# Kernel optimization log

Measured on AMD Instinct MI355X. Metric: run time of the kernel, lower is better.

The kernel has to match this reference:

```python
import jax, jax.numpy as jnp
import numpy as np

FEATURE_DIM = 1024
HEAD_NUM = 16
HIDDEN_DIM = FEATURE_DIM // HEAD_NUM


def setup_inputs() -> dict:
    key = jax.random.key(0)
    ks = jax.random.split(key, 12)
    B, S, D = 4, 2048, FEATURE_DIM
    s = 1.0 / np.sqrt(D)
    inp = {
        "query": jax.random.normal(ks[0], (B, S, D), jnp.float32),
        "key": jax.random.normal(ks[1], (B, S, D), jnp.float32),
        "value": jax.random.normal(ks[2], (B, S, D), jnp.float32),
        "mask": jax.random.randint(ks[3], (B, 1, 1, S), 0, 2, jnp.int32),
        "Wq": jax.random.normal(ks[4], (D, D), jnp.float32) * s,
        "bq": jnp.zeros((D,), jnp.float32),
        "Wk": jax.random.normal(ks[5], (D, D), jnp.float32) * s,
        "bk": jnp.zeros((D,), jnp.float32),
        "Wv": jax.random.normal(ks[6], (D, D), jnp.float32) * s,
        "bv": jnp.zeros((D,), jnp.float32),
        "Wo": jax.random.normal(ks[7], (D, D), jnp.float32) * s,
        "bo": jnp.zeros((D,), jnp.float32),
    }
    return inp


def reference(query, key, value, mask, Wq, bq, Wk, bk, Wv, bv, Wo, bo):
    B, Sq, D = query.shape
    H, Hd = HEAD_NUM, HIDDEN_DIM
    scale = jnp.sqrt(jnp.asarray(Hd, query.dtype))

    def split_heads(x):
        b, s, _ = x.shape
        return x.reshape(b, s, H, Hd).transpose(0, 2, 1, 3)  # [B,H,S,Hd]

    Q = split_heads(query @ Wq.T + bq)
    K = split_heads(key @ Wk.T + bk)
    V = split_heads(value @ Wv.T + bv)

    scores = jnp.einsum("bhqd,bhkd->bhqk", Q, K) / scale
    scores = jnp.where(mask == 0, jnp.asarray(-1e10, scores.dtype), scores)
    attn = jax.nn.softmax(scores, axis=-1)  # dropout p=0 -> identity
    h = jnp.einsum("bhqk,bhkd->bhqd", attn, V)
    h = h.transpose(0, 2, 1, 3).reshape(B, Sq, D)
    return h @ Wo.T + bo
```

## Files before the change

### kernel.cpp

```cpp
#include <hip/hip_runtime.h>
#include <hip/hip_bf16.h>
#include <cstdint>
#include <cstddef>

#define D_MODEL 1024
#define SEQ     2048
#define BATCH   4
#define NHEAD   16
#define HD      64
#define MROWS   (BATCH * SEQ)

typedef __attribute__((ext_vector_type(8))) short  short8;
typedef __attribute__((ext_vector_type(4))) float  floatx4;
typedef __attribute__((ext_vector_type(4))) unsigned short ushort4v;
typedef unsigned short u16;

__device__ __forceinline__ u16 f2bf(float x) {
    __hip_bfloat16 h = __float2bfloat16(x);
    return *(u16*)&h;
}

__device__ __forceinline__ void async_copy16(const u16* g, u16* l) {
    __builtin_amdgcn_global_load_lds(
        (const __attribute__((address_space(1))) void*)g,
        (__attribute__((address_space(3))) void*)l, 16, 0, 0);
}

__device__ __forceinline__ void cvt8(const float* s, u16* d, size_t i) {
    const float4 a = *(const float4*)(s + i);
    const float4 b = *(const float4*)(s + i + 4);
    short8 o;
    o[0] = (short)f2bf(a.x); o[1] = (short)f2bf(a.y);
    o[2] = (short)f2bf(a.z); o[3] = (short)f2bf(a.w);
    o[4] = (short)f2bf(b.x); o[5] = (short)f2bf(b.y);
    o[6] = (short)f2bf(b.z); o[7] = (short)f2bf(b.w);
    *(short8*)(d + i) = o;
}

__global__ __launch_bounds__(256) void cvt3(
    const float* __restrict__ s0, const float* __restrict__ s1,
    const float* __restrict__ s2,
    u16* __restrict__ d0, u16* __restrict__ d1, u16* __restrict__ d2)
{
    const float* s = blockIdx.y == 0 ? s0 : (blockIdx.y == 1 ? s1 : s2);
    u16*         d = blockIdx.y == 0 ? d0 : (blockIdx.y == 1 ? d1 : d2);
    cvt8(s, d, ((size_t)blockIdx.x * 256 + threadIdx.x) * 8);
}

__global__ __launch_bounds__(256) void cvt4(
    const float* __restrict__ s0, const float* __restrict__ s1,
    const float* __restrict__ s2, const float* __restrict__ s3,
    u16* __restrict__ d0, u16* __restrict__ d1,
    u16* __restrict__ d2, u16* __restrict__ d3)
{
    const float* s = blockIdx.y == 0 ? s0 : (blockIdx.y == 1 ? s1 :
                     (blockIdx.y == 2 ? s2 : s3));
    u16*         d = blockIdx.y == 0 ? d0 : (blockIdx.y == 1 ? d1 :
                     (blockIdx.y == 2 ? d2 : d3));
    cvt8(s, d, ((size_t)blockIdx.x * 256 + threadIdx.x) * 8);
}

template <int LAYOUT>
__global__ __launch_bounds__(256) void gemm_mfma(
    const u16* __restrict__ A,
    const u16* __restrict__ W,
    const float* __restrict__ bias,
    void* __restrict__ out)
{
    constexpr int K = D_MODEL;
    __shared__ __align__(16) u16 smem[16384];
    u16 (*As)[64] = (u16(*)[64])smem;
    u16 (*Ws)[64] = (u16(*)[64])(smem + 8192);

    const int bm = blockIdx.x * 128;
    const int bn = blockIdx.y * 128;
    const int t  = threadIdx.x;
    const int w  = t >> 6;
    const int l  = t & 63;
    const int li = l & 15;
    const int quad = l >> 4;
    const int wm = (w & 1) * 64;
    const int wn = (w >> 1) * 64;
    const int lrow = l >> 3;
    const int lcol = (l & 7) * 8;

    const u16* Ag = A + (size_t)bm * K;
    const u16* Wg = W + (size_t)bn * K;

    floatx4 acc[4][4];
    #pragma unroll
    for (int mi = 0; mi < 4; mi++)
        #pragma unroll
        for (int ni = 0; ni < 4; ni++) acc[mi][ni] = (floatx4){0.f,0.f,0.f,0.f};

    for (int kt = 0; kt < K; kt += 64) {
        __syncthreads();
        #pragma unroll
        for (int j = 0; j < 4; j++) {
            const int r = w * 32 + j * 8;
            async_copy16(Ag + (size_t)(r + lrow) * K + kt + lcol, &As[r][0]);
            async_copy16(Wg + (size_t)(r + lrow) * K + kt + lcol, &Ws[r][0]);
        }
        __syncthreads();

        #pragma unroll
        for (int ks = 0; ks < 2; ks++) {
            short8 af[4], bf[4];
            #pragma unroll
            for (int i = 0; i < 4; i++) {
                af[i] = *(const short8*)&As[wm + i * 16 + li][ks * 32 + quad * 8];
                bf[i] = *(const short8*)&Ws[wn + i * 16 + li][ks * 32 + quad * 8];
            }
            #pragma unroll
            for (int mi = 0; mi < 4; mi++)
                #pragma unroll
                for (int ni = 0; ni < 4; ni++)
                    acc[mi][ni] = __builtin_amdgcn_mfma_f32_16x16x32_bf16(
                        af[mi], bf[ni], acc[mi][ni], 0, 0, 0);
        }
    }

    if (LAYOUT == 3) {
        float* o = (float*)out;
        #pragma unroll
        for (int mi = 0; mi < 4; mi++)
            #pragma unroll
            for (int ni = 0; ni < 4; ni++) {
                const int c = bn + wn + ni * 16 + li;
                const float bz = bias[c];
                #pragma unroll
                for (int reg = 0; reg < 4; reg++) {
                    const int r = bm + wm + mi * 16 + quad * 4 + reg;
                    o[(size_t)r * D_MODEL + c] = acc[mi][ni][reg] + bz;
                }
            }
    } else if (LAYOUT == 0) {
        u16* o = (u16*)out;
        #pragma unroll
        for (int mi = 0; mi < 4; mi++)
            #pragma unroll
            for (int ni = 0; ni < 4; ni++) {
                const int c  = bn + wn + ni * 16 + li;
                const int h  = c >> 6;
                const int hd = c & 63;
                const float bz = bias[c];
                #pragma unroll
                for (int reg = 0; reg < 4; reg++) {
                    const int r = bm + wm + mi * 16 + quad * 4 + reg;
                    const int b = r >> 11;
                    const int s = r & (SEQ - 1);
                    o[(((size_t)(b * NHEAD + h) * SEQ) + s) * HD + hd] = f2bf(acc[mi][ni][reg] + bz);
                }
            }
    } else {
        u16 (*Ct)[128] = (u16(*)[128])smem;
        __syncthreads();
        #pragma unroll
        for (int mi = 0; mi < 4; mi++)
            #pragma unroll
            for (int ni = 0; ni < 4; ni++) {
                const int cl = wn + ni * 16 + li;
                const float bz = bias[bn + cl];
                #pragma unroll
                for (int reg = 0; reg < 4; reg++) {
                    const int rl = wm + mi * 16 + quad * 4 + reg;
                    Ct[cl][rl] = f2bf(acc[mi][ni][reg] + bz);
                }
            }
        __syncthreads();
        const int cl   = t >> 1;
        const int half = t & 1;
        const int cg = bn + cl;
        const int h  = cg >> 6;
        const int hd = cg & 63;
        const int b  = bm >> 11;
        const int s0 = (bm & (SEQ - 1)) + half * 64;
        u16* dst = (u16*)out + (((size_t)(b * NHEAD + h) * HD) + hd) * SEQ + s0;
        const short8* sp = (const short8*)&Ct[cl][half * 64];
        #pragma unroll
        for (int i = 0; i < 8; i++) ((short8*)dst)[i] = sp[i];
    }
}

#define LOG2E   1.44269504088896340736f
#define CSCALE  (0.125f * LOG2E)

__global__ __launch_bounds__(256) void attn_mfma(
    const u16* __restrict__ Q,
    const u16* __restrict__ K,
    const u16* __restrict__ Vt,
    const int* __restrict__ mask,
    u16* __restrict__ H)
{
    __shared__ __align__(16) u16 Ks[64 * 64];
    __shared__ __align__(16) u16 Vs[64 * 64];
    __shared__ __align__(16) u16 Ps[4][32][72];
    __shared__ float mc[64];

    const int bh  = blockIdx.y;
    const int b   = bh >> 4;
    const int h   = bh & 15;
    const int q0  = blockIdx.x * 128;
    const int t   = threadIdx.x;
    const int w   = t >> 6;
    const int l   = t & 63;
    const int li  = l & 15;
    const int quad  = l >> 4;
    const int lrow8 = l >> 3;
    const int gch   = (l & 7) ^ lrow8;
    const int swz   = li & 7;

    short8 qf[2][2];
    #pragma unroll
    for (int qb = 0; qb < 2; qb++) {
        const u16* Qrow = Q + ((size_t)bh * SEQ + q0 + w * 32 + qb * 16 + li) * HD;
        qf[qb][0] = *(const short8*)(Qrow + quad * 8);
        qf[qb][1] = *(const short8*)(Qrow + 32 + quad * 8);
    }

    const u16* Kbh = K  + (size_t)bh * SEQ * HD;
    const u16* Vbh = Vt + (size_t)bh * HD * SEQ;
    const int* mg  = mask + (size_t)b * SEQ;

    floatx4 oacc[4][2];
    #pragma unroll
    for (int hm = 0; hm < 4; hm++)
        #pragma unroll
        for (int qb = 0; qb < 2; qb++) oacc[hm][qb] = (floatx4){0.f,0.f,0.f,0.f};
    float rs[2] = {0.f, 0.f};

    for (int kt = 0; kt < SEQ; kt += 64) {
        __syncthreads();
        #pragma unroll
        for (int j = 0; j < 2; j++) {
            const int rb = w * 16 + j * 8;
            async_copy16(Kbh + (size_t)(kt + rb + lrow8) * HD + gch * 8, &Ks[rb * 64]);
            async_copy16(Vbh + (size_t)(rb + lrow8) * SEQ + kt + gch * 8, &Vs[rb * 64]);
        }
        if (t < 64) mc[t] = (mg[kt + t] != 0) ? -16.0f : -1.0e9f;
        __syncthreads();

        floatx4 sacc[4][2];
        #pragma unroll
        for (int kb = 0; kb < 4; kb++)
            #pragma unroll
            for (int qb = 0; qb < 2; qb++) sacc[kb][qb] = (floatx4){0.f,0.f,0.f,0.f};
        #pragma unroll
        for (int ks = 0; ks < 2; ks++) {
            short8 kf[4];
            #pragma unroll
            for (int kb = 0; kb < 4; kb++)
                kf[kb] = *(const short8*)&Ks[(kb * 16 + li) * 64 + ((ks * 4 + quad) ^ swz) * 8];
            #pragma unroll
            for (int kb = 0; kb < 4; kb++)
                #pragma unroll
                for (int qb = 0; qb < 2; qb++)
                    sacc[kb][qb] = __builtin_amdgcn_mfma_f32_16x16x32_bf16(
                        kf[kb], qf[qb][ks], sacc[kb][qb], 0, 0, 0);
        }

        #pragma unroll
        for (int kb = 0; kb < 4; kb++) {
            const float4 m4 = *(const float4*)&mc[kb * 16 + quad * 4];
            #pragma unroll
            for (int qb = 0; qb < 2; qb++) {
                const float p0 = __builtin_amdgcn_exp2f(fmaf(sacc[kb][qb][0], CSCALE, m4.x));
                const float p1 = __builtin_amdgcn_exp2f(fmaf(sacc[kb][qb][1], CSCALE, m4.y));
                const float p2 = __builtin_amdgcn_exp2f(fmaf(sacc[kb][qb][2], CSCALE, m4.z));
                const float p3 = __builtin_amdgcn_exp2f(fmaf(sacc[kb][qb][3], CSCALE, m4.w));
                rs[qb] += (p0 + p1) + (p2 + p3);
                ushort4v pk;
                pk[0] = f2bf(p0); pk[1] = f2bf(p1);
                pk[2] = f2bf(p2); pk[3] = f2bf(p3);
                *(ushort4v*)&Ps[w][qb * 16 + li][kb * 16 + quad * 4] = pk;
            }
        }

        #pragma unroll
        for (int ks = 0; ks < 2; ks++) {
            short8 pf[2];
            #pragma unroll
            for (int qb = 0; qb < 2; qb++)
                pf[qb] = *(const short8*)&Ps[w][qb * 16 + li][ks * 32 + quad * 8];
            #pragma unroll
            for (int hm = 0; hm < 4; hm++) {
                const short8 vf = *(const short8*)&Vs[(hm * 16 + li) * 64 + ((ks * 4 + quad) ^ swz) * 8];
                #pragma unroll
                for (int qb = 0; qb < 2; qb++)
                    oacc[hm][qb] = __builtin_amdgcn_mfma_f32_16x16x32_bf16(
                        vf, pf[qb], oacc[hm][qb], 0, 0, 0);
            }
        }
    }

    float linv[2];
    #pragma unroll
    for (int qb = 0; qb < 2; qb++) {
        float v = rs[qb];
        v += __shfl_xor(v, 16, 64);
        v += __shfl_xor(v, 32, 64);
        linv[qb] = 1.0f / v;
    }
    #pragma unroll
    for (int qb = 0; qb < 2; qb++) {
        const size_t row = (size_t)b * SEQ + q0 + w * 32 + qb * 16 + li;
        #pragma unroll
        for (int hm = 0; hm < 4; hm++) {
            ushort4v o;
            #pragma unroll
            for (int reg = 0; reg < 4; reg++)
                o[reg] = f2bf(oacc[hm][qb][reg] * linv[qb]);
            *(ushort4v*)&H[row * D_MODEL + h * 64 + hm * 16 + quad * 4] = o;
        }
    }
}

extern "C" void kernel_launch(void* const* d_in, const int* in_sizes, int n_in,
                              void* d_out, int out_size, void* d_ws, size_t ws_size,
                              hipStream_t stream)
{
    const float* query = (const float*)d_in[0];
    const float* key_  = (const float*)d_in[1];
    const float* value = (const float*)d_in[2];
    const int*   mask  = (const int*)  d_in[3];
    const float* Wq = (const float*)d_in[4];
    const float* bq = (const float*)d_in[5];
    const float* Wk = (const float*)d_in[6];
    const float* bk = (const float*)d_in[7];
    const float* Wv = (const float*)d_in[8];
    const float* bv = (const float*)d_in[9];
    const float* Wo = (const float*)d_in[10];
    const float* bo = (const float*)d_in[11];
    float* out = (float*)d_out;

    const size_t per = (size_t)BATCH * NHEAD * SEQ * HD;
    const size_t wsz = (size_t)D_MODEL * D_MODEL;
    u16* qb  = (u16*)d_ws;
    u16* kb  = qb  + per;
    u16* vb  = kb  + per;
    u16* Qb  = vb  + per;
    u16* Kb  = Qb  + per;
    u16* Vtb = Kb  + per;
    u16* Hb  = Vtb + per;
    u16* Wqb = Hb  + per;
    u16* Wkb = Wqb + wsz;
    u16* Wvb = Wkb + wsz;
    u16* Wob = Wvb + wsz;

    cvt3<<<dim3(per / 2048, 3), 256, 0, stream>>>(query, key_, value, qb, kb, vb);
    cvt4<<<dim3(wsz / 2048, 4), 256, 0, stream>>>(Wq, Wk, Wv, Wo, Wqb, Wkb, Wvb, Wob);

    const dim3 gg(MROWS / 128, D_MODEL / 128);
    gemm_mfma<0><<<gg, 256, 0, stream>>>(qb, Wqb, bq, Qb);
    gemm_mfma<0><<<gg, 256, 0, stream>>>(kb, Wkb, bk, Kb);
    gemm_mfma<1><<<gg, 256, 0, stream>>>(vb, Wvb, bv, Vtb);

    attn_mfma<<<dim3(SEQ / 128, BATCH * NHEAD), 256, 0, stream>>>(
        Qb, Kb, Vtb, mask, Hb);

    gemm_mfma<3><<<gg, 256, 0, stream>>>(Hb, Wob, bo, out);
}
```

Measured before the change: 393.2 us.

## Fuse fp32-to-bf16 input conversion into batched QKV GEMM and double-buffer attention K/V

Drops the separate activation conversion kernel. The Q, K and V projections now run as one batched launch over blockIdx.z, and each reads fp32 activations directly, converting them to bf16 in registers with a register-prefetch software pipeline. The attention kernel double-buffers the K/V tiles and mask in LDS so the next tile's async loads overlap the current compute, and it drops one barrier per iteration. The goal is to remove a full round trip of activation traffic and two launches, and to hide load latency in attention. The cost is more LDS in attention and register-based loads instead of direct-to-LDS copies in the GEMM.

```diff
diff --git a/kernel.cpp b/kernel.cpp
--- a/kernel.cpp
+++ b/kernel.cpp
@@ -35,16 +35,6 @@
     o[4] = (short)f2bf(b.x); o[5] = (short)f2bf(b.y);
     o[6] = (short)f2bf(b.z); o[7] = (short)f2bf(b.w);
     *(short8*)(d + i) = o;
-}
-
-__global__ __launch_bounds__(256) void cvt3(
-    const float* __restrict__ s0, const float* __restrict__ s1,
-    const float* __restrict__ s2,
-    u16* __restrict__ d0, u16* __restrict__ d1, u16* __restrict__ d2)
-{
-    const float* s = blockIdx.y == 0 ? s0 : (blockIdx.y == 1 ? s1 : s2);
-    u16*         d = blockIdx.y == 0 ? d0 : (blockIdx.y == 1 ? d1 : d2);
-    cvt8(s, d, ((size_t)blockIdx.x * 256 + threadIdx.x) * 8);
 }
 
 __global__ __launch_bounds__(256) void cvt4(
@@ -60,12 +50,148 @@
     cvt8(s, d, ((size_t)blockIdx.x * 256 + threadIdx.x) * 8);
 }
 
-template <int LAYOUT>
-__global__ __launch_bounds__(256) void gemm_mfma(
+__global__ __launch_bounds__(256) void gemm_qkv(
+    const float* __restrict__ Aq, const float* __restrict__ Ak,
+    const float* __restrict__ Av,
+    const u16* __restrict__ Wqp, const u16* __restrict__ Wkp,
+    const u16* __restrict__ Wvp,
+    const float* __restrict__ bqp, const float* __restrict__ bkp,
+    const float* __restrict__ bvp,
+    u16* __restrict__ oq, u16* __restrict__ ok, u16* __restrict__ ov)
+{
+    constexpr int K = D_MODEL;
+    __shared__ __align__(16) u16 smem[16384];
+    u16 (*As)[64] = (u16(*)[64])smem;
+    u16 (*Ws)[64] = (u16(*)[64])(smem + 8192);
+
+    const int z = blockIdx.z;
+    const float* A    = z == 0 ? Aq  : (z == 1 ? Ak  : Av);
+    const u16*   W    = z == 0 ? Wqp : (z == 1 ? Wkp : Wvp);
+    const float* bias = z == 0 ? bqp : (z == 1 ? bkp : bvp);
+    u16*         out  = z == 0 ? oq  : (z == 1 ? ok  : ov);
+
+    const int bm = blockIdx.x * 128;
+    const int bn = blockIdx.y * 128;
+    const int t  = threadIdx.x;
+    const int w  = t >> 6;
+    const int l  = t & 63;
+    const int li = l & 15;
+    const int quad = l >> 4;
+    const int wm = (w & 1) * 64;
+    const int wn = (w >> 1) * 64;
+    const int srow = w * 32 + (l >> 3);
+    const int lc8  = (l & 7) * 8;
+
+    const float* Ab = A + (size_t)bm * K;
+    const u16*   Wb = W + (size_t)bn * K;
+
+    float4 pa[4][2];
+    short8 pw[4];
+    #pragma unroll
+    for (int j = 0; j < 4; j++) {
+        const float* ap = Ab + (size_t)(srow + j * 8) * K + lc8;
+        pa[j][0] = *(const float4*)ap;
+        pa[j][1] = *(const float4*)(ap + 4);
+        pw[j] = *(const short8*)(Wb + (size_t)(srow + j * 8) * K + lc8);
+    }
+
+    floatx4 acc[4][4];
+    #pragma unroll
+    for (int mi = 0; mi < 4; mi++)
+        #pragma unroll
+        for (int ni = 0; ni < 4; ni++) acc[mi][ni] = (floatx4){0.f,0.f,0.f,0.f};
+
+    for (int kt = 0; kt < K; kt += 64) {
+        __syncthreads();
+        #pragma unroll
+        for (int j = 0; j < 4; j++) {
+            short8 av;
+            av[0] = (short)f2bf(pa[j][0].x); av[1] = (short)f2bf(pa[j][0].y);
+            av[2] = (short)f2bf(pa[j][0].z); av[3] = (short)f2bf(pa[j][0].w);
+            av[4] = (short)f2bf(pa[j][1].x); av[5] = (short)f2bf(pa[j][1].y);
+            av[6] = (short)f2bf(pa[j][1].z); av[7] = (short)f2bf(pa[j][1].w);
+            *(short8*)&As[srow + j * 8][lc8] = av;
+            *(short8*)&Ws[srow + j * 8][lc8] = pw[j];
+        }
+        __syncthreads();
+        if (kt + 64 < K) {
+            #pragma unroll
+            for (int j = 0; j < 4; j++) {
+                const float* ap = Ab + (size_t)(srow + j * 8) * K + kt + 64 + lc8;
+                pa[j][0] = *(const float4*)ap;
+                pa[j][1] = *(const float4*)(ap + 4);
+                pw[j] = *(const short8*)(Wb + (size_t)(srow + j * 8) * K + kt + 64 + lc8);
+            }
+        }
+        #pragma unroll
+        for (int ks = 0; ks < 2; ks++) {
+            short8 af[4], bf[4];
+            #pragma unroll
+            for (int i = 0; i < 4; i++) {
+                af[i] = *(const short8*)&As[wm + i * 16 + li][ks * 32 + quad * 8];
+                bf[i] = *(const short8*)&Ws[wn + i * 16 + li][ks * 32 + quad * 8];
+            }
+            #pragma unroll
+            for (int mi = 0; mi < 4; mi++)
+                #pragma unroll
+                for (int ni = 0; ni < 4; ni++)
+                    acc[mi][ni] = __builtin_amdgcn_mfma_f32_16x16x32_bf16(
+                        af[mi], bf[ni], acc[mi][ni], 0, 0, 0);
+        }
+    }
+
+    if (z < 2) {
+        #pragma unroll
+        for (int mi = 0; mi < 4; mi++)
+            #pragma unroll
+            for (int ni = 0; ni < 4; ni++) {
+                const int c  = bn + wn + ni * 16 + li;
+                const int h  = c >> 6;
+                const int hd = c & 63;
+                const float bz = bias[c];
+                #pragma unroll
+                for (int reg = 0; reg < 4; reg++) {
+                    const int r = bm + wm + mi * 16 + quad * 4 + reg;
+                    const int b = r >> 11;
+                    const int s = r & (SEQ - 1);
+                    out[(((size_t)(b * NHEAD + h) * SEQ) + s) * HD + hd] = f2bf(acc[mi][ni][reg] + bz);
+                }
+            }
+    } else {
+        u16 (*Ct)[128] = (u16(*)[128])smem;
+        __syncthreads();
+        #pragma unroll
+        for (int mi = 0; mi < 4; mi++)
+            #pragma unroll
+            for (int ni = 0; ni < 4; ni++) {
+                const int cl = wn + ni * 16 + li;
+                const float bz = bias[bn + cl];
+                #pragma unroll
+                for (int reg = 0; reg < 4; reg++) {
+                    const int rl = wm + mi * 16 + quad * 4 + reg;
+                    Ct[cl][rl] = f2bf(acc[mi][ni][reg] + bz);
+                }
+            }
+        __syncthreads();
+        const int cl   = t >> 1;
+        const int half = t & 1;
+        const int cg = bn + cl;
+        const int h  = cg >> 6;
+        const int hd = cg & 63;
+        const int b  = bm >> 11;
+        const int s0 = (bm & (SEQ - 1)) + half * 64;
+        u16* dst = out + (((size_t)(b * NHEAD + h) * HD) + hd) * SEQ + s0;
+        const short8* sp = (const short8*)&Ct[cl][half * 64];
+        #pragma unroll
+        for (int i = 0; i < 8; i++) ((short8*)dst)[i] = sp[i];
+    }
+}
+
+__global__ __launch_bounds__(256) void gemm_out(
     const u16* __restrict__ A,
     const u16* __restrict__ W,
     const float* __restrict__ bias,
-    void* __restrict__ out)
+    float* __restrict__ out)
 {
     constexpr int K = D_MODEL;
     __shared__ __align__(16) u16 smem[16384];
@@ -120,66 +246,18 @@
         }
     }
 
-    if (LAYOUT == 3) {
-        float* o = (float*)out;
-        #pragma unroll
-        for (int mi = 0; mi < 4; mi++)
-            #pragma unroll
-            for (int ni = 0; ni < 4; ni++) {
-                const int c = bn + wn + ni * 16 + li;
-                const float bz = bias[c];
-                #pragma unroll
-                for (int reg = 0; reg < 4; reg++) {
-                    const int r = bm + wm + mi * 16 + quad * 4 + reg;
-                    o[(size_t)r * D_MODEL + c] = acc[mi][ni][reg] + bz;
-                }
-            }
-    } else if (LAYOUT == 0) {
-        u16* o = (u16*)out;
-        #pragma unroll
-        for (int mi = 0; mi < 4; mi++)
-            #pragma unroll
-            for (int ni = 0; ni < 4; ni++) {
-                const int c  = bn + wn + ni * 16 + li;
-                const int h  = c >> 6;
-                const int hd = c & 63;
-                const float bz = bias[c];
-                #pragma unroll
-                for (int reg = 0; reg < 4; reg++) {
-                    const int r = bm + wm + mi * 16 + quad * 4 + reg;
-                    const int b = r >> 11;
-                    const int s = r & (SEQ - 1);
-                    o[(((size_t)(b * NHEAD + h) * SEQ) + s) * HD + hd] = f2bf(acc[mi][ni][reg] + bz);
-                }
-            }
-    } else {
-        u16 (*Ct)[128] = (u16(*)[128])smem;
-        __syncthreads();
-        #pragma unroll
-        for (int mi = 0; mi < 4; mi++)
-            #pragma unroll
-            for (int ni = 0; ni < 4; ni++) {
-                const int cl = wn + ni * 16 + li;
-                const float bz = bias[bn + cl];
-                #pragma unroll
-                for (int reg = 0; reg < 4; reg++) {
-                    const int rl = wm + mi * 16 + quad * 4 + reg;
-                    Ct[cl][rl] = f2bf(acc[mi][ni][reg] + bz);
-                }
-            }
-        __syncthreads();
-        const int cl   = t >> 1;
-        const int half = t & 1;
-        const int cg = bn + cl;
-        const int h  = cg >> 6;
-        const int hd = cg & 63;
-        const int b  = bm >> 11;
-        const int s0 = (bm & (SEQ - 1)) + half * 64;
-        u16* dst = (u16*)out + (((size_t)(b * NHEAD + h) * HD) + hd) * SEQ + s0;
-        const short8* sp = (const short8*)&Ct[cl][half * 64];
-        #pragma unroll
-        for (int i = 0; i < 8; i++) ((short8*)dst)[i] = sp[i];
-    }
+    #pragma unroll
+    for (int mi = 0; mi < 4; mi++)
+        #pragma unroll
+        for (int ni = 0; ni < 4; ni++) {
+            const int c = bn + wn + ni * 16 + li;
+            const float bz = bias[c];
+            #pragma unroll
+            for (int reg = 0; reg < 4; reg++) {
+                const int r = bm + wm + mi * 16 + quad * 4 + reg;
+                out[(size_t)r * D_MODEL + c] = acc[mi][ni][reg] + bz;
+            }
+        }
 }
 
 #define LOG2E   1.44269504088896340736f
@@ -192,10 +270,10 @@
     const int* __restrict__ mask,
     u16* __restrict__ H)
 {
-    __shared__ __align__(16) u16 Ks[64 * 64];
-    __shared__ __align__(16) u16 Vs[64 * 64];
+    __shared__ __align__(16) u16 Ks[2][64 * 64];
+    __shared__ __align__(16) u16 Vs[2][64 * 64];
     __shared__ __align__(16) u16 Ps[4][32][72];
-    __shared__ float mc[64];
+    __shared__ float mc[2][64];
 
     const int bh  = blockIdx.y;
     const int b   = bh >> 4;
@@ -229,16 +307,29 @@
         for (int qb = 0; qb < 2; qb++) oacc[hm][qb] = (floatx4){0.f,0.f,0.f,0.f};
     float rs[2] = {0.f, 0.f};
 
+    #pragma unroll
+    for (int j = 0; j < 2; j++) {
+        const int rb = w * 16 + j * 8;
+        async_copy16(Kbh + (size_t)(rb + lrow8) * HD + gch * 8, &Ks[0][rb * 64]);
+        async_copy16(Vbh + (size_t)(rb + lrow8) * SEQ + gch * 8, &Vs[0][rb * 64]);
+    }
+    if (t < 64) mc[0][t] = (mg[t] != 0) ? -16.0f : -1.0e9f;
+
+    int cur = 0;
     for (int kt = 0; kt < SEQ; kt += 64) {
         __syncthreads();
-        #pragma unroll
-        for (int j = 0; j < 2; j++) {
-            const int rb = w * 16 + j * 8;
-            async_copy16(Kbh + (size_t)(kt + rb + lrow8) * HD + gch * 8, &Ks[rb * 64]);
-            async_copy16(Vbh + (size_t)(rb + lrow8) * SEQ + kt + gch * 8, &Vs[rb * 64]);
-        }
-        if (t < 64) mc[t] = (mg[kt + t] != 0) ? -16.0f : -1.0e9f;
-        __syncthreads();
+        if (kt + 64 < SEQ) {
+            const int nb_ = cur ^ 1;
+            #pragma unroll
+            for (int j = 0; j < 2; j++) {
+                const int rb = w * 16 + j * 8;
+                async_copy16(Kbh + (size_t)(kt + 64 + rb + lrow8) * HD + gch * 8,
+                             &Ks[nb_][rb * 64]);
+                async_copy16(Vbh + (size_t)(rb + lrow8) * SEQ + kt + 64 + gch * 8,
+                             &Vs[nb_][rb * 64]);
+            }
+            if (t < 64) mc[nb_][t] = (mg[kt + 64 + t] != 0) ? -16.0f : -1.0e9f;
+        }
 
         floatx4 sacc[4][2];
         #pragma unroll
@@ -250,7 +341,7 @@
             short8 kf[4];
             #pragma unroll
             for (int kb = 0; kb < 4; kb++)
-                kf[kb] = *(const short8*)&Ks[(kb * 16 + li) * 64 + ((ks * 4 + quad) ^ swz) * 8];
+                kf[kb] = *(const short8*)&Ks[cur][(kb * 16 + li) * 64 + ((ks * 4 + quad) ^ swz) * 8];
             #pragma unroll
             for (int kb = 0; kb < 4; kb++)
                 #pragma unroll
@@ -261,7 +352,7 @@
 
         #pragma unroll
         for (int kb = 0; kb < 4; kb++) {
-            const float4 m4 = *(const float4*)&mc[kb * 16 + quad * 4];
+            const float4 m4 = *(const float4*)&mc[cur][kb * 16 + quad * 4];
             #pragma unroll
             for (int qb = 0; qb < 2; qb++) {
                 const float p0 = __builtin_amdgcn_exp2f(fmaf(sacc[kb][qb][0], CSCALE, m4.x));
@@ -284,13 +375,14 @@
                 pf[qb] = *(const short8*)&Ps[w][qb * 16 + li][ks * 32 + quad * 8];
             #pragma unroll
             for (int hm = 0; hm < 4; hm++) {
-                const short8 vf = *(const short8*)&Vs[(hm * 16 + li) * 64 + ((ks * 4 + quad) ^ swz) * 8];
+                const short8 vf = *(const short8*)&Vs[cur][(hm * 16 + li) * 64 + ((ks * 4 + quad) ^ swz) * 8];
                 #pragma unroll
                 for (int qb = 0; qb < 2; qb++)
                     oacc[hm][qb] = __builtin_amdgcn_mfma_f32_16x16x32_bf16(
                         vf, pf[qb], oacc[hm][qb], 0, 0, 0);
             }
         }
+        cur ^= 1;
     }
 
     float linv[2];
@@ -335,10 +427,7 @@
 
     const size_t per = (size_t)BATCH * NHEAD * SEQ * HD;
     const size_t wsz = (size_t)D_MODEL * D_MODEL;
-    u16* qb  = (u16*)d_ws;
-    u16* kb  = qb  + per;
-    u16* vb  = kb  + per;
-    u16* Qb  = vb  + per;
+    u16* Qb  = (u16*)d_ws;
     u16* Kb  = Qb  + per;
     u16* Vtb = Kb  + per;
     u16* Hb  = Vtb + per;
@@ -347,16 +436,15 @@
     u16* Wvb = Wkb + wsz;
     u16* Wob = Wvb + wsz;
 
-    cvt3<<<dim3(per / 2048, 3), 256, 0, stream>>>(query, key_, value, qb, kb, vb);
-    cvt4<<<dim3(wsz / 2048, 4), 256, 0, stream>>>(Wq, Wk, Wv, Wo, Wqb, Wkb, Wvb, Wob);
-
-    const dim3 gg(MROWS / 128, D_MODEL / 128);
-    gemm_mfma<0><<<gg, 256, 0, stream>>>(qb, Wqb, bq, Qb);
-    gemm_mfma<0><<<gg, 256, 0, stream>>>(kb, Wkb, bk, Kb);
-    gemm_mfma<1><<<gg, 256, 0, stream>>>(vb, Wvb, bv, Vtb);
+    cvt4<<<dim3(wsz / 2048, 4), 256, 0, stream>>>(Wq, Wk, Wv, Wo,
+                                                  Wqb, Wkb, Wvb, Wob);
+
+    gemm_qkv<<<dim3(MROWS / 128, D_MODEL / 128, 3), 256, 0, stream>>>(
+        query, key_, value, Wqb, Wkb, Wvb, bq, bk, bv, Qb, Kb, Vtb);
 
     attn_mfma<<<dim3(SEQ / 128, BATCH * NHEAD), 256, 0, stream>>>(
         Qb, Kb, Vtb, mask, Hb);
 
-    gemm_mfma<3><<<gg, 256, 0, stream>>>(Hb, Wob, bo, out);
-}
+    gemm_out<<<dim3(MROWS / 128, D_MODEL / 128), 256, 0, stream>>>(
+        Hb, Wob, bo, out);
+}
```

After: 373.9 us. 4.9% less time.
